# Performance work log

Hardware: AMD Instinct MI355X
Metric: run time of the kernel (lower is better)

Reference implementation:

```python
import jax, jax.numpy as jnp
import numpy as np

N = 50000   # nodes
E = 600000  # edges per edge_index
G = 64      # graphs in batch
H = 128     # hidden_neurons == n_node_features
EPS = 1e-12 # F.normalize eps


def sage(x, edge, Wl, bl, Wr, norm):
    # PyG SAGEConv (aggr='mean'): out_i = lin_l(mean_{j->i} x_j) + lin_r(x_i)
    src, dst = edge[0], edge[1]
    s = jax.ops.segment_sum(x[src], dst, num_segments=N)          # [N,H]
    cnt = jax.ops.segment_sum(jnp.ones((edge.shape[1],), x.dtype), dst, num_segments=N)
    agg = s / jnp.maximum(cnt, 1.0)[:, None]
    out = agg @ Wl + bl + x @ Wr
    if norm:  # F.normalize(out, p=2, dim=-1)
        n = jnp.linalg.norm(out, axis=-1, keepdims=True)
        out = out / jnp.maximum(n, EPS)
    return out


def setup_inputs() -> dict:
    key = jax.random.key(0)
    ks = jax.random.split(key, 40)
    sc = 1.0 / np.sqrt(H)
    d = {}
    d["x"] = jax.random.normal(ks[0], (N, H), jnp.float32)
    d["eic"] = jax.random.randint(ks[1], (2, E), 0, N, dtype=jnp.int32)
    d["eid"] = jax.random.randint(ks[2], (2, E), 0, N, dtype=jnp.int32)
    d["eit"] = jax.random.randint(ks[3], (2, E), 0, N, dtype=jnp.int32)
    d["batch"] = jnp.sort(jax.random.randint(ks[4], (N,), 0, G, dtype=jnp.int32))
    i = 5
    for c in ["c1", "c2", "c3", "c4", "c5"]:
        d[c + "_Wl"] = jax.random.normal(ks[i], (H, H), jnp.float32) * sc; i += 1
        d[c + "_bl"] = jnp.zeros((H,), jnp.float32)
        d[c + "_Wr"] = jax.random.normal(ks[i], (H, H), jnp.float32) * sc; i += 1
    d["l0_W"] = jax.random.normal(ks[i], (H, H), jnp.float32) * sc; i += 1
    d["l0_b"] = jnp.zeros((H,), jnp.float32)
    d["l1_W"] = jax.random.normal(ks[i], (H, H), jnp.float32) * sc; i += 1
    d["l1_b"] = jnp.zeros((H,), jnp.float32)
    d["head_W"] = jax.random.normal(ks[i], (H, 1), jnp.float32) * sc; i += 1
    d["head_b"] = jnp.zeros((1,), jnp.float32)
    return d


def reference(x, eic, eid, eit, batch,
              c1_Wl, c1_bl, c1_Wr, c2_Wl, c2_bl, c2_Wr, c3_Wl, c3_bl, c3_Wr,
              c4_Wl, c4_bl, c4_Wr, c5_Wl, c5_bl, c5_Wr,
              l0_W, l0_b, l1_W, l1_b, head_W, head_b):
    h = sage(x, eid, c1_Wl, c1_bl, c1_Wr, True)
    for _ in range(2):  # it_b4_dest, shared conv2 weights
        h = sage(h, eic, c2_Wl, c2_bl, c2_Wr, True)
    h = sage(h, eit, c3_Wl, c3_bl, c3_Wr, False)  # conv3 normalize=False
    h = sage(h, eid, c4_Wl, c4_bl, c4_Wr, True)
    for _ in range(2):  # it_aft_dest, shared conv5 weights
        h = sage(h, eic, c5_Wl, c5_bl, c5_Wr, True)
    g = jax.ops.segment_sum(h, batch, num_segments=G)  # global_add_pool -> [G,H]
    g = jax.nn.relu(g @ l0_W + l0_b)
    g = jax.nn.relu(g @ l1_W + l1_b)
    return g @ head_W + head_b  # [G,1]
```

## Files before the change

kernel.cpp:

```cpp
#include <hip/hip_runtime.h>
#include <hip/hip_bf16.h>


constexpr int N_NODES = 50000;
constexpr int NE      = 600000;
constexpr int H       = 128;
constexpr int NG      = 64;
constexpr int N3      = 3 * N_NODES;

constexpr int NB   = (N3 + 1023) >> 10;
constexpr int EPB  = 2048;
constexpr int BPS  = (NE + EPB - 1) / EPB;
constexpr int CAP2 = 19456;

typedef __attribute__((ext_vector_type(8))) short short8;
typedef __attribute__((ext_vector_type(4))) float f32x4;

__device__ __forceinline__ ushort f2bf(float f) {
    uint x = __float_as_uint(f);
    return (ushort)((x + 0x7FFFu + ((x >> 16) & 1u)) >> 16);
}
__device__ __forceinline__ float bf2f(ushort u) {
    return __uint_as_float(((uint)u) << 16);
}


__global__ __launch_bounds__(256) void k_bucketize(
    const int* __restrict__ e0, const int* __restrict__ e1,
    const int* __restrict__ e2, int* __restrict__ gcnt,
    int* __restrict__ rcnt, int2* __restrict__ bucket) {
    __shared__ int hist[NB];
    __shared__ int basearr[NB];
    __shared__ int cur[NB];
    __shared__ int gposs[NB];
    __shared__ int2 stage[EPB];
    __shared__ int dstoff[EPB];

    int t = threadIdx.x;
    int s = blockIdx.x / BPS;
    int w = blockIdx.x - s * BPS;
    const int* ep = (s == 0 ? e0 : (s == 1 ? e1 : e2));
    int eBase = w * EPB;
    int m = NE - eBase;
    if (m > EPB) m = EPB;

    for (int i = t; i < NB; i += 256) hist[i] = 0;
    __syncthreads();

    int myk[EPB / 256], mys[EPB / 256];
#pragma unroll
    for (int k = 0; k < EPB / 256; ++k) {
        int i = t + 256 * k;
        if (i < m) {
            int d   = ep[NE + eBase + i];
            int src = ep[eBase + i];
            int key = s * N_NODES + d;
            myk[k] = key; mys[k] = src;
            atomicAdd(&hist[key >> 10], 1);
        } else {
            myk[k] = -1;
        }
    }
    __syncthreads();

    if (t == 0) {
        int run = 0;
        for (int b = 0; b < NB; ++b) { basearr[b] = run; run += hist[b]; }
    }
    __syncthreads();

    if (t < NB) {
        int h = hist[t];
        int p = (h + 7) & ~7;
        gposs[t] = p ? atomicAdd(&gcnt[t], p) : 0;
        if (h) atomicAdd(&rcnt[t], h);
        cur[t] = 0;
    }
    __syncthreads();

#pragma unroll
    for (int k = 0; k < EPB / 256; ++k) {
        if (myk[k] >= 0) {
            int b  = myk[k] >> 10;
            int sl = atomicAdd(&cur[b], 1);
            int p  = basearr[b] + sl;
            stage[p]  = make_int2(myk[k], mys[k]);
            dstoff[p] = b * CAP2 + gposs[b] + sl;
        }
    }
    __syncthreads();

    for (int i = t; i < m; i += 256) bucket[dstoff[i]] = stage[i];
    for (int i = t; i < NB * 8; i += 256) {
        int b = i >> 3, j = i & 7;
        int h = hist[b];
        int p = (h + 7) & ~7;
        if (h + j < p)
            bucket[(size_t)b * CAP2 + gposs[b] + h + j] = make_int2(-1, 0);
    }
}


__global__ __launch_bounds__(512) void k_scatter2(const int2* __restrict__ bucket,
                                                  const int* __restrict__ gcnt,
                                                  const int* __restrict__ rcnt,
                                                  int* __restrict__ ptr,
                                                  int* __restrict__ adj) {
    int b = blockIdx.x;
    int base = b << 10;
    int nk = N3 - base;
    if (nk > 1024) nk = 1024;
    __shared__ int lh[1024];
    __shared__ int lsum[512];
    __shared__ int lfill[1024];
    __shared__ int bb;
    int t = threadIdx.x;

    int rv = (t < NB) ? rcnt[t] : 0;
    lsum[t] = rv;
    __syncthreads();
    for (int off = 1; off < 512; off <<= 1) {
        int u = (t >= off) ? lsum[t - off] : 0;
        __syncthreads();
        if (t >= off) lsum[t] += u;
        __syncthreads();
    }
    if (t == b) bb = lsum[t] - rv;
    if (b == 0 && t == 0) ptr[N3] = 3 * NE;
    for (int i = t; i < 1024; i += 512) lh[i] = 0;
    __syncthreads();

    int c = gcnt[b];
    const int2* seg = bucket + (size_t)b * CAP2;
    for (int i = t; i < c; i += 512) {
        int k = seg[i].x;
        if (k >= 0) atomicAdd(&lh[k - base], 1);
    }
    __syncthreads();
    int v0 = lh[t * 2], v1 = lh[t * 2 + 1];
    int ts = v0 + v1;
    lsum[t] = ts;
    __syncthreads();
    for (int off = 1; off < 512; off <<= 1) {
        int u = (t >= off) ? lsum[t - off] : 0;
        __syncthreads();
        if (t >= off) lsum[t] += u;
        __syncthreads();
    }
    int ex = lsum[t] - ts + bb;
    int e0 = ex, e1 = ex + v0;
    if (t * 2     < nk) { ptr[base + t * 2]     = e0; lfill[t * 2]     = e0; }
    if (t * 2 + 1 < nk) { ptr[base + t * 2 + 1] = e1; lfill[t * 2 + 1] = e1; }
    __syncthreads();
    for (int i = t; i < c; i += 512) {
        int2 ed = seg[i];
        if (ed.x >= 0) {
            int pos = atomicAdd(&lfill[ed.x - base], 1);
            adj[pos] = ed.y;
        }
    }
}


__global__ void k_prep(const float* __restrict__ x, ushort* __restrict__ hi,
                       ushort* __restrict__ lo, int* __restrict__ zmem,
                       const float* W0l, const float* W0r, const float* W1l,
                       const float* W1r, const float* W2l, const float* W2r,
                       const float* W3l, const float* W3r, const float* W4l,
                       const float* W4r, ushort* __restrict__ Bpk) {
    int bid = blockIdx.x;
    int t   = threadIdx.x;
    if (bid < 640) {
        int idx = bid * 256 + t;
        if (idx >= 5 * 32768) return;
        int c = idx >> 15, r = idx & 32767;
        const float* Wl = (c == 0 ? W0l : c == 1 ? W1l : c == 2 ? W2l : c == 3 ? W3l : W4l);
        const float* Wr = (c == 0 ? W0r : c == 1 ? W1r : c == 2 ? W2r : c == 3 ? W3r : W4r);
        int n = r & 255, k = r >> 8;
        float w = (n < H) ? Wl[k * H + n] : Wr[k * H + (n - H)];
        int q = k >> 5, g = (k >> 3) & 3, j = k & 7;
        int off = ((q * 4 + g) * 256 + n) * 8 + j;
        ushort h = f2bf(w);
        ushort* bh = Bpk + (size_t)c * 65536;
        bh[off]         = h;
        bh[32768 + off] = f2bf(w - bf2f(h));
        return;
    }
    int tid = (bid - 640) * 256 + t;
    if (tid < NG * H + 2 * NB) zmem[tid] = 0;
    size_t i = (size_t)tid * 4;
    if (i >= (size_t)N_NODES * H) return;
    float4 v = *(const float4*)(x + i);
    ushort4 h, l;
    h.x = f2bf(v.x); l.x = f2bf(v.x - bf2f(h.x));
    h.y = f2bf(v.y); l.y = f2bf(v.y - bf2f(h.y));
    h.z = f2bf(v.z); l.z = f2bf(v.z - bf2f(h.z));
    h.w = f2bf(v.w); l.w = f2bf(v.w - bf2f(h.w));
    *(ushort4*)(hi + i) = h;
    *(ushort4*)(lo + i) = l;
}


__global__ __launch_bounds__(256) void k_gemm_mfma(
    const ushort* __restrict__ Ahi, const ushort* __restrict__ Alo,
    const ushort* __restrict__ Bh, const ushort* __restrict__ Bl,
    ushort* __restrict__ z, ushort* __restrict__ yb) {
    __shared__ ushort AshF[2 * 64 * 128];
    int t = threadIdx.x;
    int rowBase = blockIdx.x * 64;
    {
        int wslot = t & ~63;
        int lane  = t & 63;
#pragma unroll
        for (int i = 0; i < 8; ++i) {
            int sbase = i * 256 + wslot;
            int S     = sbase + lane;
            int plane = S >> 10;
            int row   = (S >> 4) & 63;
            int pc    = S & 15;
            int grow  = rowBase + row;
            if (grow > N_NODES - 1) grow = N_NODES - 1;
            const ushort* Ap  = plane ? Alo : Ahi;
            const ushort* src = Ap + (size_t)grow * H + ((pc ^ (row & 15)) << 3);
            ushort* ldst = AshF + (size_t)sbase * 8;
            __builtin_amdgcn_global_load_lds(
                (const __attribute__((address_space(1))) void*)src,
                (__attribute__((address_space(3))) void*)ldst, 16, 0, 0);
        }
    }
    __syncthreads();

    int wave = t >> 6, lane = t & 63;
    int m16 = lane & 15, q4 = lane >> 4;
    int n0 = wave * 64;

    f32x4 acc[4][4];
#pragma unroll
    for (int r = 0; r < 4; ++r)
#pragma unroll
        for (int c = 0; c < 4; ++c) {
            acc[r][c][0] = 0.f; acc[r][c][1] = 0.f;
            acc[r][c][2] = 0.f; acc[r][c][3] = 0.f;
        }

    for (int q = 0; q < 4; ++q) {
        short8 bh_[4], bl_[4], ah_[4], al_[4];
#pragma unroll
        for (int c = 0; c < 4; ++c) {
            int boff = ((q * 4 + q4) * 256 + n0 + c * 16 + m16) * 8;
            bh_[c] = *(const short8*)(Bh + boff);
            bl_[c] = *(const short8*)(Bl + boff);
        }
#pragma unroll
        for (int r = 0; r < 4; ++r) {
            int roff = ((r * 16 + m16) << 7) + (((q * 4 + q4) ^ m16) << 3);
            ah_[r] = *(const short8*)&AshF[roff];
            al_[r] = *(const short8*)&AshF[8192 + roff];
        }
#pragma unroll
        for (int r = 0; r < 4; ++r)
#pragma unroll
            for (int c = 0; c < 4; ++c) {
                acc[r][c] = __builtin_amdgcn_mfma_f32_16x16x32_bf16(
                    ah_[r], bh_[c], acc[r][c], 0, 0, 0);
                acc[r][c] = __builtin_amdgcn_mfma_f32_16x16x32_bf16(
                    ah_[r], bl_[c], acc[r][c], 0, 0, 0);
                acc[r][c] = __builtin_amdgcn_mfma_f32_16x16x32_bf16(
                    al_[r], bh_[c], acc[r][c], 0, 0, 0);
            }
    }

#pragma unroll
    for (int r = 0; r < 4; ++r)
#pragma unroll
        for (int c = 0; c < 4; ++c) {
            int col = n0 + c * 16 + m16;
            ushort* op = (col < H) ? (z + col) : (yb + (col - H));
#pragma unroll
            for (int j = 0; j < 4; ++j) {
                int gr = rowBase + r * 16 + q4 * 4 + j;
                if (gr < N_NODES) op[(size_t)gr * H] = f2bf(acc[r][c][j]);
            }
        }
}


__global__ __launch_bounds__(256, 8) void k_aggnorm(
    const ushort* __restrict__ z, const ushort* __restrict__ yb,
    const int* __restrict__ ptr, const int* __restrict__ adj,
    const float* __restrict__ bl,
    ushort* __restrict__ hhi, ushort* __restrict__ hlo, int norm) {
    int gtid = blockIdx.x * blockDim.x + threadIdx.x;
    int node = gtid >> 4;
    int sl   = threadIdx.x & 15;
    if (node >= N_NODES) return;
    int beg = ptr[node], end = ptr[node + 1];
    int deg = end - beg;
    const ushort* zrow = z + sl * 8;
    float a[8];
#pragma unroll
    for (int k = 0; k < 8; ++k) a[k] = 0.f;

    for (int base = 0; base < deg; base += 16) {
        int m = deg - base;
        if (m > 16) m = 16;
        int idx = (sl < m) ? adj[beg + base + sl] : 0;
#pragma unroll
        for (int half = 0; half < 2; ++half) {
            int mh = m - half * 8;
            if (mh <= 0) continue;
            if (mh > 8) mh = 8;
            int hb = half * 8;
            short8 v[8];
#pragma unroll
            for (int jj = 0; jj < 8; ++jj) {
                int nj = __shfl(idx, hb + jj, 16);
                if (jj < mh) v[jj] = *(const short8*)(zrow + (size_t)nj * H);
            }
            if (mh == 8) {
#pragma unroll
                for (int k = 0; k < 8; ++k)
                    a[k] += ((bf2f((ushort)v[0][k]) + bf2f((ushort)v[1][k])) +
                             (bf2f((ushort)v[2][k]) + bf2f((ushort)v[3][k]))) +
                            ((bf2f((ushort)v[4][k]) + bf2f((ushort)v[5][k])) +
                             (bf2f((ushort)v[6][k]) + bf2f((ushort)v[7][k])));
            } else if (mh >= 4) {
#pragma unroll
                for (int k = 0; k < 8; ++k)
                    a[k] += (bf2f((ushort)v[0][k]) + bf2f((ushort)v[1][k])) +
                            (bf2f((ushort)v[2][k]) + bf2f((ushort)v[3][k]));
                if (mh > 4) {
#pragma unroll
                    for (int k = 0; k < 8; ++k) a[k] += bf2f((ushort)v[4][k]);
                }
                if (mh > 5) {
#pragma unroll
                    for (int k = 0; k < 8; ++k) a[k] += bf2f((ushort)v[5][k]);
                }
                if (mh > 6) {
#pragma unroll
                    for (int k = 0; k < 8; ++k) a[k] += bf2f((ushort)v[6][k]);
                }
            } else {
                if (mh > 0) {
#pragma unroll
                    for (int k = 0; k < 8; ++k) a[k] += bf2f((ushort)v[0][k]);
                }
                if (mh > 1) {
#pragma unroll
                    for (int k = 0; k < 8; ++k) a[k] += bf2f((ushort)v[1][k]);
                }
                if (mh > 2) {
#pragma unroll
                    for (int k = 0; k < 8; ++k) a[k] += bf2f((ushort)v[2][k]);
                }
            }
        }
    }

    float inv = 1.0f / (float)(deg > 1 ? deg : 1);
    short8 yv = *(const short8*)(yb + (size_t)node * H + sl * 8);
    float4 bva = *(const float4*)(bl + sl * 8);
    float4 bvb = *(const float4*)(bl + sl * 8 + 4);
    float vv[8];
    vv[0] = a[0] * inv + bva.x + bf2f((ushort)yv[0]);
    vv[1] = a[1] * inv + bva.y + bf2f((ushort)yv[1]);
    vv[2] = a[2] * inv + bva.z + bf2f((ushort)yv[2]);
    vv[3] = a[3] * inv + bva.w + bf2f((ushort)yv[3]);
    vv[4] = a[4] * inv + bvb.x + bf2f((ushort)yv[4]);
    vv[5] = a[5] * inv + bvb.y + bf2f((ushort)yv[5]);
    vv[6] = a[6] * inv + bvb.z + bf2f((ushort)yv[6]);
    vv[7] = a[7] * inv + bvb.w + bf2f((ushort)yv[7]);
    if (norm) {
        float ss = 0.f;
#pragma unroll
        for (int k = 0; k < 8; ++k) ss += vv[k] * vv[k];
#pragma unroll
        for (int mm = 1; mm < 16; mm <<= 1) ss += __shfl_xor(ss, mm, 16);
        float n2 = 1.0f / fmaxf(sqrtf(ss), 1e-12f);
#pragma unroll
        for (int k = 0; k < 8; ++k) vv[k] *= n2;
    }
    short8 ho, lo8;
#pragma unroll
    for (int k = 0; k < 8; ++k) {
        ushort hh = f2bf(vv[k]);
        ho[k]  = (short)hh;
        lo8[k] = (short)f2bf(vv[k] - bf2f(hh));
    }
    *(short8*)(hhi + (size_t)node * H + sl * 8) = ho;
    *(short8*)(hlo + (size_t)node * H + sl * 8) = lo8;
}


constexpr int POOL_ROWS = 64;

__global__ void k_pool(const ushort* __restrict__ hhi, const ushort* __restrict__ hlo,
                       const int* __restrict__ batch, float* __restrict__ g) {
    int col = threadIdx.x;
    int r0 = blockIdx.x * POOL_ROWS;
    int r1 = r0 + POOL_ROWS;
    if (r1 > N_NODES) r1 = N_NODES;
    if (r0 >= N_NODES) return;
    float acc = 0.f;
    int cur = batch[r0];
    int r = r0;
    for (; r + 4 <= r1; r += 4) {
        float v0 = bf2f(hhi[(size_t)r * H + col])       + bf2f(hlo[(size_t)r * H + col]);
        float v1 = bf2f(hhi[(size_t)(r + 1) * H + col]) + bf2f(hlo[(size_t)(r + 1) * H + col]);
        float v2 = bf2f(hhi[(size_t)(r + 2) * H + col]) + bf2f(hlo[(size_t)(r + 2) * H + col]);
        float v3 = bf2f(hhi[(size_t)(r + 3) * H + col]) + bf2f(hlo[(size_t)(r + 3) * H + col]);
        int b3 = batch[r + 3];
        if (b3 == cur) {
            acc += (v0 + v1) + (v2 + v3);
        } else {
            int b0 = batch[r], b1 = batch[r + 1], b2 = batch[r + 2];
            if (b0 != cur) { atomicAdd(&g[cur * H + col], acc); acc = 0.f; cur = b0; }
            acc += v0;
            if (b1 != cur) { atomicAdd(&g[cur * H + col], acc); acc = 0.f; cur = b1; }
            acc += v1;
            if (b2 != cur) { atomicAdd(&g[cur * H + col], acc); acc = 0.f; cur = b2; }
            acc += v2;
            if (b3 != cur) { atomicAdd(&g[cur * H + col], acc); acc = 0.f; cur = b3; }
            acc += v3;
        }
    }
    for (; r < r1; ++r) {
        int b = batch[r];
        if (b != cur) { atomicAdd(&g[cur * H + col], acc); acc = 0.f; cur = b; }
        acc += bf2f(hhi[(size_t)r * H + col]) + bf2f(hlo[(size_t)r * H + col]);
    }
    atomicAdd(&g[cur * H + col], acc);
}


__global__ void k_mlp(const float* __restrict__ g, const float* __restrict__ W0,
                      const float* __restrict__ b0, const float* __restrict__ W1,
                      const float* __restrict__ b1, const float* __restrict__ Wh,
                      const float* __restrict__ bh, float* __restrict__ out) {
    int gi = blockIdx.x;
    int t  = threadIdx.x;
    __shared__ float buf0[H];
    __shared__ float buf1[H];
    __shared__ float red[2];

    float acc = b0[t];
    for (int k = 0; k < H; ++k) acc += g[gi * H + k] * W0[k * H + t];
    buf0[t] = fmaxf(acc, 0.f);
    __syncthreads();

    acc = b1[t];
    for (int k = 0; k < H; ++k) acc += buf0[k] * W1[k * H + t];
    buf1[t] = fmaxf(acc, 0.f);
    __syncthreads();

    float p = buf1[t] * Wh[t];
    for (int m = 1; m < 64; m <<= 1) p += __shfl_xor(p, m, 64);
    if ((t & 63) == 0) red[t >> 6] = p;
    __syncthreads();
    if (t == 0) out[gi] = red[0] + red[1] + bh[0];
}


extern "C" void kernel_launch(void* const* d_in, const int* in_sizes, int n_in,
                              void* d_out, int out_size, void* d_ws, size_t ws_size,
                              hipStream_t stream) {
    const float* x     = (const float*)d_in[0];
    const int*   eic   = (const int*)d_in[1];
    const int*   eid   = (const int*)d_in[2];
    const int*   eit   = (const int*)d_in[3];
    const int*   batch = (const int*)d_in[4];
    const float* cW[5][3];
    for (int c = 0; c < 5; ++c) {
        cW[c][0] = (const float*)d_in[5 + c * 3 + 0];
        cW[c][1] = (const float*)d_in[5 + c * 3 + 1];
        cW[c][2] = (const float*)d_in[5 + c * 3 + 2];
    }
    const float* l0_W = (const float*)d_in[20];
    const float* l0_b = (const float*)d_in[21];
    const float* l1_W = (const float*)d_in[22];
    const float* l1_b = (const float*)d_in[23];
    const float* hd_W = (const float*)d_in[24];
    const float* hd_b = (const float*)d_in[25];
    float* outp = (float*)d_out;

    const size_t NH = (size_t)N_NODES * H;
    ushort* Ahi = (ushort*)d_ws;
    ushort* Alo = Ahi + NH;
    ushort* zb  = Alo + NH;
    ushort* yb  = zb + NH;
    ushort* Bpk = yb + NH;
    float*  gbuf = (float*)(Bpk + 5 * 2 * 32768);
    int* gcnt = (int*)(gbuf + (size_t)NG * H);
    int* rcnt = gcnt + NB;
    int* ptr_all = rcnt + NB;
    int* adj_all = ptr_all + (N3 + 1);
    int2* bucket = (int2*)zb;

    dim3 b256(256);

    k_prep<<<dim3(640 + (int)(NH / 1024)), b256, 0, stream>>>(
        x, Ahi, Alo, (int*)gbuf,
        cW[0][0], cW[0][2], cW[1][0], cW[1][2], cW[2][0], cW[2][2],
        cW[3][0], cW[3][2], cW[4][0], cW[4][2], Bpk);

    k_bucketize<<<dim3(3 * BPS), b256, 0, stream>>>(eic, eid, eit, gcnt, rcnt, bucket);
    k_scatter2<<<dim3(NB), dim3(512), 0, stream>>>(bucket, gcnt, rcnt, ptr_all, adj_all);

    const int L_set[7]  = {1, 0, 0, 2, 1, 0, 0};
    const int L_conv[7] = {0, 1, 1, 2, 3, 4, 4};
    const int L_norm[7] = {1, 1, 1, 0, 1, 1, 1};

    dim3 gAgg((N_NODES * 16 + 255) / 256);
    dim3 gGemm((N_NODES + 63) / 64);

    for (int L = 0; L < 7; ++L) {
        int s = L_set[L], c = L_conv[L];
        const ushort* Bh = Bpk + (size_t)c * 65536;
        const ushort* Bl = Bh + 32768;
        k_gemm_mfma<<<gGemm, b256, 0, stream>>>(Ahi, Alo, Bh, Bl, zb, yb);
        k_aggnorm<<<gAgg, b256, 0, stream>>>(zb, yb, ptr_all + s * N_NODES, adj_all,
                                             cW[c][1], Ahi, Alo, L_norm[L]);
    }

    k_pool<<<dim3((N_NODES + POOL_ROWS - 1) / POOL_ROWS), dim3(H), 0, stream>>>(
        Ahi, Alo, batch, gbuf);
    k_mlp<<<dim3(NG), dim3(H), 0, stream>>>(gbuf, l0_W, l0_b, l1_W, l1_b, hd_W, hd_b,
                                            outp);
}
```

Before: 509.7 us.

## Fuse aggregation/normalize with next layer GEMM via shared-memory hand-off

```diff
diff --git a/kernel.cpp b/kernel.cpp
--- a/kernel.cpp
+++ b/kernel.cpp
@@ -276,6 +276,176 @@
         for (int c = 0; c < 4; ++c) {
             int col = n0 + c * 16 + m16;
             ushort* op = (col < H) ? (z + col) : (yb + (col - H));
+#pragma unroll
+            for (int j = 0; j < 4; ++j) {
+                int gr = rowBase + r * 16 + q4 * 4 + j;
+                if (gr < N_NODES) op[(size_t)gr * H] = f2bf(acc[r][c][j]);
+            }
+        }
+}
+
+
+__global__ __launch_bounds__(256) void k_fused(
+    const ushort* __restrict__ zin, const ushort* __restrict__ yin,
+    ushort* __restrict__ zout, ushort* __restrict__ yout,
+    const int* __restrict__ ptr, const int* __restrict__ adj,
+    const float* __restrict__ bl,
+    const ushort* __restrict__ Bh, const ushort* __restrict__ Blw,
+    int norm) {
+    __shared__ ushort Ash[2][64][136];
+    int t = threadIdx.x;
+    int rowBase = blockIdx.x * 64;
+    int sl = t & 15;
+    int nic = t >> 4;
+
+    for (int c4 = 0; c4 < 4; ++c4) {
+        int row = c4 * 16 + nic;
+        int node = rowBase + row;
+        if (node > N_NODES - 1) node = N_NODES - 1;
+        int beg = ptr[node], end = ptr[node + 1];
+        int deg = end - beg;
+        const ushort* zrow = zin + sl * 8;
+        float a[8];
+#pragma unroll
+        for (int k = 0; k < 8; ++k) a[k] = 0.f;
+
+        for (int base = 0; base < deg; base += 16) {
+            int m = deg - base;
+            if (m > 16) m = 16;
+            int idx = (sl < m) ? adj[beg + base + sl] : 0;
+#pragma unroll
+            for (int half = 0; half < 2; ++half) {
+                int mh = m - half * 8;
+                if (mh <= 0) continue;
+                if (mh > 8) mh = 8;
+                int hb = half * 8;
+                short8 v[8];
+#pragma unroll
+                for (int jj = 0; jj < 8; ++jj) {
+                    int nj = __shfl(idx, hb + jj, 16);
+                    if (jj < mh) v[jj] = *(const short8*)(zrow + (size_t)nj * H);
+                }
+                if (mh == 8) {
+#pragma unroll
+                    for (int k = 0; k < 8; ++k)
+                        a[k] += ((bf2f((ushort)v[0][k]) + bf2f((ushort)v[1][k])) +
+                                 (bf2f((ushort)v[2][k]) + bf2f((ushort)v[3][k]))) +
+                                ((bf2f((ushort)v[4][k]) + bf2f((ushort)v[5][k])) +
+                                 (bf2f((ushort)v[6][k]) + bf2f((ushort)v[7][k])));
+                } else if (mh >= 4) {
+#pragma unroll
+                    for (int k = 0; k < 8; ++k)
+                        a[k] += (bf2f((ushort)v[0][k]) + bf2f((ushort)v[1][k])) +
+                                (bf2f((ushort)v[2][k]) + bf2f((ushort)v[3][k]));
+                    if (mh > 4) {
+#pragma unroll
+                        for (int k = 0; k < 8; ++k) a[k] += bf2f((ushort)v[4][k]);
+                    }
+                    if (mh > 5) {
+#pragma unroll
+                        for (int k = 0; k < 8; ++k) a[k] += bf2f((ushort)v[5][k]);
+                    }
+                    if (mh > 6) {
+#pragma unroll
+                        for (int k = 0; k < 8; ++k) a[k] += bf2f((ushort)v[6][k]);
+                    }
+                } else {
+                    if (mh > 0) {
+#pragma unroll
+                        for (int k = 0; k < 8; ++k) a[k] += bf2f((ushort)v[0][k]);
+                    }
+                    if (mh > 1) {
+#pragma unroll
+                        for (int k = 0; k < 8; ++k) a[k] += bf2f((ushort)v[1][k]);
+                    }
+                    if (mh > 2) {
+#pragma unroll
+                        for (int k = 0; k < 8; ++k) a[k] += bf2f((ushort)v[2][k]);
+                    }
+                }
+            }
+        }
+
+        float inv = 1.0f / (float)(deg > 1 ? deg : 1);
+        short8 yv = *(const short8*)(yin + (size_t)node * H + sl * 8);
+        float4 bva = *(const float4*)(bl + sl * 8);
+        float4 bvb = *(const float4*)(bl + sl * 8 + 4);
+        float vv[8];
+        vv[0] = a[0] * inv + bva.x + bf2f((ushort)yv[0]);
+        vv[1] = a[1] * inv + bva.y + bf2f((ushort)yv[1]);
+        vv[2] = a[2] * inv + bva.z + bf2f((ushort)yv[2]);
+        vv[3] = a[3] * inv + bva.w + bf2f((ushort)yv[3]);
+        vv[4] = a[4] * inv + bvb.x + bf2f((ushort)yv[4]);
+        vv[5] = a[5] * inv + bvb.y + bf2f((ushort)yv[5]);
+        vv[6] = a[6] * inv + bvb.z + bf2f((ushort)yv[6]);
+        vv[7] = a[7] * inv + bvb.w + bf2f((ushort)yv[7]);
+        if (norm) {
+            float ss = 0.f;
+#pragma unroll
+            for (int k = 0; k < 8; ++k) ss += vv[k] * vv[k];
+#pragma unroll
+            for (int mm = 1; mm < 16; mm <<= 1) ss += __shfl_xor(ss, mm, 16);
+            float n2 = 1.0f / fmaxf(sqrtf(ss), 1e-12f);
+#pragma unroll
+            for (int k = 0; k < 8; ++k) vv[k] *= n2;
+        }
+        short8 ho, lo8;
+#pragma unroll
+        for (int k = 0; k < 8; ++k) {
+            ushort hh = f2bf(vv[k]);
+            ho[k]  = (short)hh;
+            lo8[k] = (short)f2bf(vv[k] - bf2f(hh));
+        }
+        *(short8*)&Ash[0][row][sl * 8] = ho;
+        *(short8*)&Ash[1][row][sl * 8] = lo8;
+    }
+    __syncthreads();
+
+    int wave = t >> 6, lane = t & 63;
+    int m16 = lane & 15, q4 = lane >> 4;
+    int n0 = wave * 64;
+
+    f32x4 acc[4][4];
+#pragma unroll
+    for (int r = 0; r < 4; ++r)
+#pragma unroll
+        for (int c = 0; c < 4; ++c) {
+            acc[r][c][0] = 0.f; acc[r][c][1] = 0.f;
+            acc[r][c][2] = 0.f; acc[r][c][3] = 0.f;
+        }
+
+    for (int q = 0; q < 4; ++q) {
+        short8 bh_[4], bl_[4], ah_[4], al_[4];
+#pragma unroll
+        for (int c = 0; c < 4; ++c) {
+            int boff = ((q * 4 + q4) * 256 + n0 + c * 16 + m16) * 8;
+            bh_[c] = *(const short8*)(Bh + boff);
+            bl_[c] = *(const short8*)(Blw + boff);
+        }
+#pragma unroll
+        for (int r = 0; r < 4; ++r) {
+            ah_[r] = *(const short8*)&Ash[0][r * 16 + m16][q * 32 + q4 * 8];
+            al_[r] = *(const short8*)&Ash[1][r * 16 + m16][q * 32 + q4 * 8];
+        }
+#pragma unroll
+        for (int r = 0; r < 4; ++r)
+#pragma unroll
+            for (int c = 0; c < 4; ++c) {
+                acc[r][c] = __builtin_amdgcn_mfma_f32_16x16x32_bf16(
+                    ah_[r], bh_[c], acc[r][c], 0, 0, 0);
+                acc[r][c] = __builtin_amdgcn_mfma_f32_16x16x32_bf16(
+                    ah_[r], bl_[c], acc[r][c], 0, 0, 0);
+                acc[r][c] = __builtin_amdgcn_mfma_f32_16x16x32_bf16(
+                    al_[r], bh_[c], acc[r][c], 0, 0, 0);
+            }
+    }
+
+#pragma unroll
+    for (int r = 0; r < 4; ++r)
+#pragma unroll
+        for (int c = 0; c < 4; ++c) {
+            int col = n0 + c * 16 + m16;
+            ushort* op = (col < H) ? (zout + col) : (yout + (col - H));
 #pragma unroll
             for (int j = 0; j < 4; ++j) {
                 int gr = rowBase + r * 16 + q4 * 4 + j;
@@ -487,15 +657,17 @@
     const size_t NH = (size_t)N_NODES * H;
     ushort* Ahi = (ushort*)d_ws;
     ushort* Alo = Ahi + NH;
-    ushort* zb  = Alo + NH;
-    ushort* yb  = zb + NH;
-    ushort* Bpk = yb + NH;
+    ushort* zb0 = Alo + NH;
+    ushort* yb0 = zb0 + NH;
+    ushort* zb1 = yb0 + NH;
+    ushort* yb1 = zb1 + NH;
+    ushort* Bpk = yb1 + NH;
     float*  gbuf = (float*)(Bpk + 5 * 2 * 32768);
     int* gcnt = (int*)(gbuf + (size_t)NG * H);
     int* rcnt = gcnt + NB;
     int* ptr_all = rcnt + NB;
     int* adj_all = ptr_all + (N3 + 1);
-    int2* bucket = (int2*)zb;
+    int2* bucket = (int2*)zb0;
 
     dim3 b256(256);
 
@@ -511,17 +683,28 @@
     const int L_conv[7] = {0, 1, 1, 2, 3, 4, 4};
     const int L_norm[7] = {1, 1, 1, 0, 1, 1, 1};
 
+    dim3 gGemm((N_NODES + 63) / 64);
     dim3 gAgg((N_NODES * 16 + 255) / 256);
-    dim3 gGemm((N_NODES + 63) / 64);
-
-    for (int L = 0; L < 7; ++L) {
-        int s = L_set[L], c = L_conv[L];
-        const ushort* Bh = Bpk + (size_t)c * 65536;
+
+    k_gemm_mfma<<<gGemm, b256, 0, stream>>>(Ahi, Alo, Bpk + (size_t)L_conv[0] * 65536,
+                                            Bpk + (size_t)L_conv[0] * 65536 + 32768,
+                                            zb0, yb0);
+
+    for (int L = 0; L < 6; ++L) {
+        ushort* zi = (L & 1) ? zb1 : zb0;
+        ushort* yi = (L & 1) ? yb1 : yb0;
+        ushort* zo = (L & 1) ? zb0 : zb1;
+        ushort* yo = (L & 1) ? yb0 : yb1;
+        const ushort* Bh = Bpk + (size_t)L_conv[L + 1] * 65536;
         const ushort* Bl = Bh + 32768;
-        k_gemm_mfma<<<gGemm, b256, 0, stream>>>(Ahi, Alo, Bh, Bl, zb, yb);
-        k_aggnorm<<<gAgg, b256, 0, stream>>>(zb, yb, ptr_all + s * N_NODES, adj_all,
-                                             cW[c][1], Ahi, Alo, L_norm[L]);
-    }
+        k_fused<<<gGemm, b256, 0, stream>>>(zi, yi, zo, yo,
+                                            ptr_all + L_set[L] * N_NODES, adj_all,
+                                            cW[L_conv[L]][1], Bh, Bl, L_norm[L]);
+    }
+
+    k_aggnorm<<<gAgg, b256, 0, stream>>>(zb0, yb0, ptr_all + L_set[6] * N_NODES,
+                                         adj_all, cW[L_conv[6]][1], Ahi, Alo,
+                                         L_norm[6]);
 
     k_pool<<<dim3((N_NODES + POOL_ROWS - 1) / POOL_ROWS), dim3(H), 0, stream>>>(
         Ahi, Alo, batch, gbuf);
```

New measurement: 553.3 us. 8.6% more time.
